# Performance work log

Hardware: AMD Instinct MI355X
Metric: run time of the kernel (lower is better)

## Reference

```python
import jax, jax.numpy as jnp
import numpy as np

N, E, D_IN, H, D_OUT = 50000, 1600000, 256, 128, 64


def setup_inputs() -> dict:
    key = jax.random.key(0)
    ks = jax.random.split(key, 8)
    x = jax.random.normal(ks[0], (N, D_IN), dtype=jnp.float32)
    edge_index = jax.random.randint(ks[1], (2, E), 0, N, dtype=jnp.int64)
    W1 = jax.random.normal(ks[2], (D_IN, H), dtype=jnp.float32) / np.float32(np.sqrt(D_IN))
    b1 = jnp.zeros((H,), jnp.float32)
    W2 = jax.random.normal(ks[3], (H, H), dtype=jnp.float32) / np.float32(np.sqrt(H))
    b2 = jnp.zeros((H,), jnp.float32)
    W3 = jax.random.normal(ks[4], (H, D_OUT), dtype=jnp.float32) / np.float32(np.sqrt(H))
    b3 = jnp.zeros((D_OUT,), jnp.float32)
    return {"x": x, "W1": W1, "b1": b1, "W2": W2, "b2": b2, "W3": W3, "b3": b3,
            "edge_index": edge_index}


def reference(x, W1, b1, W2, b2, W3, b3, edge_index):
    n = x.shape[0]
    # GCN: add self-loops, symmetric normalization D^{-1/2}(A+I)D^{-1/2}
    loop = jnp.arange(n, dtype=edge_index.dtype)
    src = jnp.concatenate([edge_index[0], loop])
    dst = jnp.concatenate([edge_index[1], loop])
    deg = jax.ops.segment_sum(jnp.ones_like(dst, x.dtype), dst, num_segments=n)
    dinv = jnp.where(deg > 0, jax.lax.rsqrt(deg), 0.0).astype(x.dtype)
    norm = dinv[src] * dinv[dst]  # [E+N]

    def gcn_layer(h, W, b):
        h = h @ W                                   # [N, F_out]
        msg = norm[:, None] * h[src]                # gather + scale, [E+N, F_out]
        return jax.ops.segment_sum(msg, dst, num_segments=n) + b

    h = jax.nn.relu(gcn_layer(x, W1, b1))
    h = jax.nn.relu(gcn_layer(h, W2, b2))
    return gcn_layer(h, W3, b3)
```

## Files before the change

kernel.cpp:

```cpp
#include <hip/hip_runtime.h>


constexpr int DIN = 256;
constexpr int HID = 128;
constexpr int DOUT = 64;
constexpr int MAXB = 1024;
constexpr int BSH = 6;
constexpr int EPB = 8192;

typedef unsigned short ushort_t;
typedef unsigned int uint_t;
typedef __attribute__((ext_vector_type(8))) short bf16x8;
typedef __attribute__((ext_vector_type(4))) float f32x4;

__device__ inline ushort_t f2bf(float f) {
  uint_t u = __float_as_uint(f);
  u += 0x7FFF + ((u >> 16) & 1);
  return (ushort_t)(u >> 16);
}
__device__ inline float bf2f(ushort_t b) {
  return __uint_as_float(((uint_t)b) << 16);
}

template <int SH>
__device__ inline uint_t ldrow32(const ushort_t* __restrict__ t, int c, uint_t lb) {
  return *(const uint_t*)((const char*)t + ((((uint_t)c) << SH) | lb));
}


__device__ inline void wprep_one(const float* __restrict__ W, ushort_t* __restrict__ Bhi,
                                 ushort_t* __restrict__ Blo, int K, int F, int i) {
  int k = i / F, nn = i % F;
  int t = nn >> 4, s = k >> 5, q = (k >> 3) & 3, j = k & 7;
  int lane = q * 16 + (nn & 15);
  int KS = K >> 5;
  size_t idx = (((size_t)t * KS + s) * 64 + (size_t)lane) * 8 + j;
  float w = W[i];
  ushort_t h = f2bf(w);
  float r = w - bf2f(h);
  Bhi[idx] = h;
  Blo[idx] = f2bf(r);
}


__global__ __launch_bounds__(256) void initprep_kernel(
    int* __restrict__ bucket_total, int iblocks,
    const float* __restrict__ W1, ushort_t* __restrict__ W1hi, ushort_t* __restrict__ W1lo,
    const float* __restrict__ W2, ushort_t* __restrict__ W2hi, ushort_t* __restrict__ W2lo,
    const float* __restrict__ W3, ushort_t* __restrict__ W3hi, ushort_t* __restrict__ W3lo) {
  if ((int)blockIdx.x < iblocks) {
    int i = blockIdx.x * 256 + threadIdx.x;
    if (i < MAXB) bucket_total[i] = 0;
  } else {
    int idx = ((int)blockIdx.x - iblocks) * 256 + threadIdx.x;
    constexpr int S1 = DIN * HID;
    constexpr int S2 = S1 + HID * HID;
    constexpr int S3 = S2 + HID * DOUT;
    if (idx < S1) wprep_one(W1, W1hi, W1lo, DIN, HID, idx);
    else if (idx < S2) wprep_one(W2, W2hi, W2lo, HID, HID, idx - S1);
    else if (idx < S3) wprep_one(W3, W3hi, W3lo, HID, DOUT, idx - S2);
  }
}


__global__ __launch_bounds__(256) void bin_kernel(const int* __restrict__ dst, int e,
    int nbuckets, int* __restrict__ bucket_total, int* __restrict__ block_base) {
  __shared__ int h[MAXB];
  int tid = threadIdx.x;
  for (int i = tid; i < nbuckets; i += 256) h[i] = 0;
  __syncthreads();
  int base = blockIdx.x * EPB;
  int end = min(base + EPB, e);
  for (int i = base + tid; i < end; i += 256) atomicAdd(&h[dst[i] >> BSH], 1);
  __syncthreads();
  for (int i = tid; i < nbuckets; i += 256) {
    int v = h[i];
    if (v) block_base[(size_t)blockIdx.x * nbuckets + i] = atomicAdd(&bucket_total[i], v);
  }
}


__global__ __launch_bounds__(256) void scan_buckets_kernel(const int* __restrict__ total,
    int* __restrict__ base, int nb) {
  __shared__ int sums[256];
  int t = threadIdx.x;
  int a[4];
  int ls = 0;
#pragma unroll
  for (int k = 0; k < 4; ++k) {
    int idx = t * 4 + k;
    a[k] = (idx < nb) ? total[idx] : 0;
    ls += a[k];
  }
  sums[t] = ls;
  __syncthreads();
  for (int off = 1; off < 256; off <<= 1) {
    int u = (t >= off) ? sums[t - off] : 0;
    __syncthreads();
    sums[t] += u;
    __syncthreads();
  }
  int run = sums[t] - ls;
#pragma unroll
  for (int k = 0; k < 4; ++k) {
    int idx = t * 4 + k;
    if (idx < nb) base[idx] = run;
    run += a[k];
  }
  if (t == 255) base[nb] = sums[255];
}


template <int K, int F, bool SCALE>
__device__ inline void gemm_mfma_dev(const float* __restrict__ X,
    const ushort_t* __restrict__ Bhi, const ushort_t* __restrict__ Blo,
    const float* __restrict__ dinv, ushort_t* __restrict__ T, int n, int bid) {
  constexpr int NT = F / 16;
  constexpr int KS = K / 32;
  int wave = threadIdx.x >> 6;
  int lane = threadIdx.x & 63;
  int q = lane >> 4;
  int m = lane & 15;
  int arow = bid * 64 + wave * 16 + m;
  bool valid = arow < n;
  const float* xrow = X + (size_t)arow * K;

  f32x4 acc[NT];
#pragma unroll
  for (int t = 0; t < NT; ++t) acc[t] = (f32x4){0.f, 0.f, 0.f, 0.f};

  for (int s = 0; s < KS; ++s) {
    float av[8];
    if (valid) {
      float4 u0 = *(const float4*)(xrow + s * 32 + q * 8);
      float4 u1 = *(const float4*)(xrow + s * 32 + q * 8 + 4);
      av[0] = u0.x; av[1] = u0.y; av[2] = u0.z; av[3] = u0.w;
      av[4] = u1.x; av[5] = u1.y; av[6] = u1.z; av[7] = u1.w;
    } else {
#pragma unroll
      for (int j = 0; j < 8; ++j) av[j] = 0.f;
    }
    bf16x8 ahi, alo;
#pragma unroll
    for (int j = 0; j < 8; ++j) {
      ushort_t h = f2bf(av[j]);
      ahi[j] = (short)h;
      alo[j] = (short)f2bf(av[j] - bf2f(h));
    }
#pragma unroll
    for (int t = 0; t < NT; ++t) {
      size_t boff = (((size_t)t * KS + s) * 64 + (size_t)lane) * 8;
      bf16x8 bh = *(const bf16x8*)(Bhi + boff);
      bf16x8 bl = *(const bf16x8*)(Blo + boff);
      acc[t] = __builtin_amdgcn_mfma_f32_16x16x32_bf16(ahi, bh, acc[t], 0, 0, 0);
      acc[t] = __builtin_amdgcn_mfma_f32_16x16x32_bf16(alo, bh, acc[t], 0, 0, 0);
      acc[t] = __builtin_amdgcn_mfma_f32_16x16x32_bf16(ahi, bl, acc[t], 0, 0, 0);
    }
  }

  int orow_base = bid * 64 + wave * 16 + q * 4;
#pragma unroll
  for (int r = 0; r < 4; ++r) {
    int orow = orow_base + r;
    if (orow >= n) continue;
    float sc = SCALE ? dinv[orow] : 1.0f;
    ushort_t* trow = T + (size_t)orow * F + m;
#pragma unroll
    for (int t = 0; t < NT; ++t) trow[t * 16] = f2bf(sc * acc[t][r]);
  }
}


__global__ __launch_bounds__(256) void fusedA2_kernel(
    const float* __restrict__ X, const ushort_t* __restrict__ Bhi,
    const ushort_t* __restrict__ Blo, ushort_t* __restrict__ T, int n, int gblocks,
    const int* __restrict__ src, const int* __restrict__ dst,
    const int* __restrict__ bucket_base, const int* __restrict__ block_base,
    uint_t* __restrict__ binned, int e, int nbuckets) {
  if ((int)blockIdx.x < gblocks) {
    gemm_mfma_dev<DIN, HID, false>(X, Bhi, Blo, nullptr, T, n, blockIdx.x);
  } else {
    __shared__ int rkh[MAXB];
    __shared__ int cbase[MAXB];
    int tid = threadIdx.x;
    int blk = (int)blockIdx.x - gblocks;
    for (int i = tid; i < nbuckets; i += 256) {
      rkh[i] = 0;
      cbase[i] = bucket_base[i] + block_base[(size_t)blk * nbuckets + i];
    }
    __syncthreads();
    int base = blk * EPB;
    int end = min(base + EPB, e);
    for (int i = base + tid; i < end; i += 256) {
      int d = dst[i];
      int s = src[i];
      int b = d >> BSH;
      int r = atomicAdd(&rkh[b], 1);
      binned[cbase[b] + r] = ((uint_t)d << 16) | (uint_t)s;
    }
  }
}


__global__ __launch_bounds__(256) void csr_kernel(const uint_t* __restrict__ binned,
    const int* __restrict__ bucket_base, int n, int* __restrict__ row_start,
    int* __restrict__ deg, float* __restrict__ dinv, int* __restrict__ col,
    ushort_t* __restrict__ Ta) {
  __shared__ int cnt[64];
  __shared__ int rk[64];
  __shared__ int rs[64];
  __shared__ float sdinv[64];
  __shared__ int ebs[2];
  int tid = threadIdx.x;
  int b = blockIdx.x;
  int node0 = b << BSH;
  if (tid < 64) { cnt[tid] = 0; rk[tid] = 0; }
  if (tid == 0) { ebs[0] = bucket_base[b]; ebs[1] = bucket_base[b + 1]; }
  __syncthreads();
  int ebase = ebs[0];
  int esz = ebs[1] - ebase;
  for (int i = tid; i < esz; i += 256)
    atomicAdd(&cnt[(int)(binned[ebase + i] >> 16) - node0], 1);
  __syncthreads();
  if (tid < 64) {
    int v = cnt[tid];
    int inc = v;
#pragma unroll
    for (int off = 1; off < 64; off <<= 1) {
      int u = __shfl_up(inc, off, 64);
      if (tid >= off) inc += u;
    }
    rs[tid] = inc - v;
    float di = rsqrtf((float)(v + 1));
    sdinv[tid] = di;
    int node = node0 + tid;
    if (node < n) {
      deg[node] = v + 1;
      dinv[node] = di;
      row_start[node] = ebase + (inc - v);
    }
  }
  __syncthreads();
  for (int i = tid; i < esz; i += 256) {
    uint_t p = binned[ebase + i];
    int l = (int)(p >> 16) - node0;
    int r = atomicAdd(&rk[l], 1);
    col[ebase + rs[l] + r] = (int)(p & 0xFFFFu);
  }
  int nrows = min(64, n - node0);
  if (nrows > 0) {
    uint4* tw = (uint4*)Ta + ((size_t)node0 << 4);
    int nv4 = nrows << 4;
    for (int i = tid; i < nv4; i += 256) {
      float sc = sdinv[i >> 4];
      uint4 w = tw[i];
      uint_t ww[4] = {w.x, w.y, w.z, w.w};
#pragma unroll
      for (int j = 0; j < 4; ++j) {
        float lo = sc * bf2f((ushort_t)(ww[j] & 0xFFFF));
        float hi = sc * bf2f((ushort_t)(ww[j] >> 16));
        ww[j] = (uint_t)f2bf(lo) | ((uint_t)f2bf(hi) << 16);
      }
      w.x = ww[0]; w.y = ww[1]; w.z = ww[2]; w.w = ww[3];
      tw[i] = w;
    }
  }
}


template <int FOUT>
__global__ __launch_bounds__(256) void spmm_gemm_kernel(
    const ushort_t* __restrict__ t, const int* __restrict__ row_start,
    const int* __restrict__ deg, const int* __restrict__ col,
    const float* __restrict__ dinv, const float* __restrict__ bias,
    const ushort_t* __restrict__ Bhi, const ushort_t* __restrict__ Blo,
    ushort_t* __restrict__ Tout, int n) {
  constexpr int FIN = 128;
  constexpr int NPB = 8;
  constexpr int LDW = FIN + 4;
  __shared__ float agg[16][LDW];
  int wave = threadIdx.x >> 6;
  int lane = threadIdx.x & 63;
  int tid = threadIdx.x;
  int nb0 = (int)blockIdx.x * NPB;
  uint_t lb = (uint_t)lane << 2;

  {
    float* z = &agg[8][0];
    for (int i = tid; i < 8 * LDW; i += 256) z[i] = 0.f;
  }

  {
    int ln0 = wave * 2;
    int n0 = nb0 + ln0;
    int n1 = n0 + 1;
    bool h0 = n0 < n, h1 = n1 < n;
    int rs0 = h0 ? row_start[n0] : 0, e0 = h0 ? deg[n0] - 1 : 0;
    int rs1 = h1 ? row_start[n1] : 0, e1 = h1 ? deg[n1] - 1 : 0;
    float di0 = h0 ? dinv[n0] : 0.f;
    float di1 = h1 ? dinv[n1] : 0.f;
    float bx = bias[2 * lane], by = bias[2 * lane + 1];
    float ax0 = 0.f, ay0 = 0.f, ax1 = 0.f, ay1 = 0.f;
    if (h0) {
      uint_t s0 = ldrow32<8>(t, n0, lb);
      ax0 = bf2f((ushort_t)(s0 & 0xFFFF)); ay0 = bf2f((ushort_t)(s0 >> 16));
    }
    if (h1) {
      uint_t s1 = ldrow32<8>(t, n1, lb);
      ax1 = bf2f((ushort_t)(s1 & 0xFFFF)); ay1 = bf2f((ushort_t)(s1 >> 16));
    }
    int p0 = rs0, q0 = rs0 + e0;
    int p1 = rs1, q1 = rs1 + e1;
    while (p0 + 8 <= q0 && p1 + 8 <= q1) {
      int c[16];
      uint_t v[16];
#pragma unroll
      for (int j = 0; j < 8; ++j) { c[j] = col[p0 + j]; c[8 + j] = col[p1 + j]; }
#pragma unroll
      for (int j = 0; j < 16; ++j) v[j] = ldrow32<8>(t, c[j], lb);
#pragma unroll
      for (int j = 0; j < 8; ++j) {
        ax0 += bf2f((ushort_t)(v[j] & 0xFFFF));
        ay0 += bf2f((ushort_t)(v[j] >> 16));
        ax1 += bf2f((ushort_t)(v[8 + j] & 0xFFFF));
        ay1 += bf2f((ushort_t)(v[8 + j] >> 16));
      }
      p0 += 8; p1 += 8;
    }
    while (p0 + 4 <= q0 && p1 + 4 <= q1) {
      int c[8];
      uint_t v[8];
#pragma unroll
      for (int j = 0; j < 4; ++j) { c[j] = col[p0 + j]; c[4 + j] = col[p1 + j]; }
#pragma unroll
      for (int j = 0; j < 8; ++j) v[j] = ldrow32<8>(t, c[j], lb);
#pragma unroll
      for (int j = 0; j < 4; ++j) {
        ax0 += bf2f((ushort_t)(v[j] & 0xFFFF));
        ay0 += bf2f((ushort_t)(v[j] >> 16));
        ax1 += bf2f((ushort_t)(v[4 + j] & 0xFFFF));
        ay1 += bf2f((ushort_t)(v[4 + j] >> 16));
      }
      p0 += 4; p1 += 4;
    }
    for (; p0 + 4 <= q0; p0 += 4) {
      int c[4]; uint_t v[4];
#pragma unroll
      for (int j = 0; j < 4; ++j) c[j] = col[p0 + j];
#pragma unroll
      for (int j = 0; j < 4; ++j) v[j] = ldrow32<8>(t, c[j], lb);
#pragma unroll
      for (int j = 0; j < 4; ++j) {
        ax0 += bf2f((ushort_t)(v[j] & 0xFFFF)); ay0 += bf2f((ushort_t)(v[j] >> 16));
      }
    }
    for (; p0 < q0; ++p0) {
      uint_t v = ldrow32<8>(t, col[p0], lb);
      ax0 += bf2f((ushort_t)(v & 0xFFFF)); ay0 += bf2f((ushort_t)(v >> 16));
    }
    for (; p1 + 4 <= q1; p1 += 4) {
      int c[4]; uint_t v[4];
#pragma unroll
      for (int j = 0; j < 4; ++j) c[j] = col[p1 + j];
#pragma unroll
      for (int j = 0; j < 4; ++j) v[j] = ldrow32<8>(t, c[j], lb);
#pragma unroll
      for (int j = 0; j < 4; ++j) {
        ax1 += bf2f((ushort_t)(v[j] & 0xFFFF)); ay1 += bf2f((ushort_t)(v[j] >> 16));
      }
    }
    for (; p1 < q1; ++p1) {
      uint_t v = ldrow32<8>(t, col[p1], lb);
      ax1 += bf2f((ushort_t)(v & 0xFFFF)); ay1 += bf2f((ushort_t)(v >> 16));
    }
    float2 o0, o1;
    o0.x = h0 ? fmaxf(fmaf(di0, ax0, bx), 0.f) : 0.f;
    o0.y = h0 ? fmaxf(fmaf(di0, ay0, by), 0.f) : 0.f;
    o1.x = h1 ? fmaxf(fmaf(di1, ax1, bx), 0.f) : 0.f;
    o1.y = h1 ? fmaxf(fmaf(di1, ay1, by), 0.f) : 0.f;
    *(float2*)&agg[ln0][2 * lane] = o0;
    *(float2*)&agg[ln0 + 1][2 * lane] = o1;
  }
  __syncthreads();

  constexpr int NT = FOUT / 16;
  constexpr int KS = FIN / 32;
  constexpr int NTW = NT / 4;
  int q = lane >> 4, m = lane & 15;
  f32x4 acc[NTW];
#pragma unroll
  for (int tt = 0; tt < NTW; ++tt) acc[tt] = (f32x4){0.f, 0.f, 0.f, 0.f};
  const float* arow = &agg[m][0];
#pragma unroll
  for (int s = 0; s < KS; ++s) {
    float4 u0 = *(const float4*)(arow + s * 32 + q * 8);
    float4 u1 = *(const float4*)(arow + s * 32 + q * 8 + 4);
    float av[8];
    av[0] = u0.x; av[1] = u0.y; av[2] = u0.z; av[3] = u0.w;
    av[4] = u1.x; av[5] = u1.y; av[6] = u1.z; av[7] = u1.w;
    bf16x8 ahi, alo;
#pragma unroll
    for (int j = 0; j < 8; ++j) {
      ushort_t h = f2bf(av[j]);
      ahi[j] = (short)h;
      alo[j] = (short)f2bf(av[j] - bf2f(h));
    }
#pragma unroll
    for (int tt = 0; tt < NTW; ++tt) {
      int tg = wave * NTW + tt;
      size_t boff = (((size_t)tg * KS + s) * 64 + (size_t)lane) * 8;
      bf16x8 bh = *(const bf16x8*)(Bhi + boff);
      bf16x8 bl = *(const bf16x8*)(Blo + boff);
      acc[tt] = __builtin_amdgcn_mfma_f32_16x16x32_bf16(ahi, bh, acc[tt], 0, 0, 0);
      acc[tt] = __builtin_amdgcn_mfma_f32_16x16x32_bf16(alo, bh, acc[tt], 0, 0, 0);
      acc[tt] = __builtin_amdgcn_mfma_f32_16x16x32_bf16(ahi, bl, acc[tt], 0, 0, 0);
    }
  }
#pragma unroll
  for (int r = 0; r < 4; ++r) {
    int row = q * 4 + r;
    if (row >= NPB) continue;
    int orow = nb0 + row;
    if (orow >= n) continue;
    float sc = dinv[orow];
    ushort_t* trow = Tout + (size_t)orow * FOUT + m;
#pragma unroll
    for (int tt = 0; tt < NTW; ++tt)
      trow[(wave * NTW + tt) * 16] = f2bf(sc * acc[tt][r]);
  }
}


__global__ __launch_bounds__(256) void spmm64_kernel(const ushort_t* __restrict__ t,
    const int* __restrict__ row_start, const int* __restrict__ deg,
    const int* __restrict__ col, const float* __restrict__ dinv,
    const float* __restrict__ bias, float* __restrict__ out, int n) {
  int gw = (int)((blockIdx.x * 256u + threadIdx.x) >> 6);
  int lane = threadIdx.x & 63;
  int half = lane >> 5;
  int hl = lane & 31;
  int n0 = gw * 2;
  if (n0 >= n) return;
  int node = n0 + half;
  bool valid = node < n;
  int vnode = valid ? node : n0;
  int rs = row_start[vnode];
  int e  = valid ? (deg[vnode] - 1) : 0;
  float di = dinv[vnode];
  uint_t lb = (uint_t)hl << 2;

  uint_t su = ldrow32<7>(t, vnode, lb);
  float ax = bf2f((ushort_t)(su & 0xFFFF));
  float ay = bf2f((ushort_t)(su >> 16));

  for (int k = 0; k < e; k += 8) {
    int c[8];
    uint_t v[8];
#pragma unroll
    for (int j = 0; j < 8; ++j) c[j] = col[(k + j) < e ? (rs + k + j) : rs];
#pragma unroll
    for (int j = 0; j < 8; ++j) v[j] = ldrow32<7>(t, c[j], lb);
#pragma unroll
    for (int j = 0; j < 8; ++j) {
      if ((k + j) < e) {
        ax += bf2f((ushort_t)(v[j] & 0xFFFF));
        ay += bf2f((ushort_t)(v[j] >> 16));
      }
    }
  }
  if (valid) {
    float bx = bias[2 * hl], by = bias[2 * hl + 1];
    ax = fmaf(di, ax, bx);
    ay = fmaf(di, ay, by);
    float2 o;
    o.x = ax;
    o.y = ay;
    *(float2*)(out + (size_t)node * DOUT + 2 * hl) = o;
  }
}


extern "C" void kernel_launch(void* const* d_in, const int* in_sizes, int n_in,
                              void* d_out, int out_size, void* d_ws, size_t ws_size,
                              hipStream_t stream) {
  const float* x  = (const float*)d_in[0];
  const float* W1 = (const float*)d_in[1];
  const float* b1 = (const float*)d_in[2];
  const float* W2 = (const float*)d_in[3];
  const float* b2 = (const float*)d_in[4];
  const float* W3 = (const float*)d_in[5];
  const float* b3 = (const float*)d_in[6];
  const int* ei   = (const int*)d_in[7];

  int n = in_sizes[0] / DIN;
  int e = in_sizes[7] / 2;
  const int* src = ei;
  const int* dst = ei + e;

  char* ws = (char*)d_ws;
  size_t off = 0;
  auto alloc = [&](size_t bytes) -> void* {
    off = (off + 255) & ~(size_t)255;
    void* p = ws + off;
    off += bytes;
    return p;
  };
  int nbuckets = (n + 63) >> BSH;
  int nbin = (e + EPB - 1) / EPB;

  int*      bucket_total = (int*)alloc((size_t)MAXB * 4);
  int*      bucket_base  = (int*)alloc((size_t)(MAXB + 1) * 4);
  int*      block_base   = (int*)alloc((size_t)nbin * nbuckets * 4);
  uint_t*   binned       = (uint_t*)alloc((size_t)e * 4);
  int*      deg          = (int*)alloc((size_t)n * 4);
  float*    dinv         = (float*)alloc((size_t)n * 4);
  int*      row_start    = (int*)alloc((size_t)n * 4);
  int*      col          = (int*)alloc((size_t)e * 4);
  ushort_t* Ta           = (ushort_t*)alloc((size_t)n * HID * 2);
  ushort_t* Tb           = (ushort_t*)alloc((size_t)n * HID * 2);
  ushort_t* W1hi         = (ushort_t*)alloc((size_t)DIN * HID * 2);
  ushort_t* W1lo         = (ushort_t*)alloc((size_t)DIN * HID * 2);
  ushort_t* W2hi         = (ushort_t*)alloc((size_t)HID * HID * 2);
  ushort_t* W2lo         = (ushort_t*)alloc((size_t)HID * HID * 2);
  ushort_t* W3hi         = (ushort_t*)alloc((size_t)HID * DOUT * 2);
  ushort_t* W3lo         = (ushort_t*)alloc((size_t)HID * DOUT * 2);
  (void)ws_size;

  int gemm_blocks = (n + 63) / 64;
  int sg_blocks = (n + 7) / 8;
  int nwaves = (n + 1) / 2;
  int spmm_blocks = (nwaves + 3) / 4;
  constexpr int WPREP_TOTAL = DIN * HID + HID * HID + HID * DOUT;
  int wblocks = (WPREP_TOTAL + 255) / 256;
  int iblocks = MAXB / 256;

  initprep_kernel<<<iblocks + wblocks, 256, 0, stream>>>(
      bucket_total, iblocks,
      W1, W1hi, W1lo, W2, W2hi, W2lo, W3, W3hi, W3lo);
  bin_kernel<<<nbin, 256, 0, stream>>>(dst, e, nbuckets, bucket_total, block_base);
  scan_buckets_kernel<<<1, 256, 0, stream>>>(bucket_total, bucket_base, nbuckets);
  fusedA2_kernel<<<gemm_blocks + nbin, 256, 0, stream>>>(
      x, W1hi, W1lo, Ta, n, gemm_blocks,
      src, dst, bucket_base, block_base, binned, e, nbuckets);
  csr_kernel<<<nbuckets, 256, 0, stream>>>(binned, bucket_base, n, row_start,
                                           deg, dinv, col, Ta);

  spmm_gemm_kernel<HID><<<sg_blocks, 256, 0, stream>>>(
      Ta, row_start, deg, col, dinv, b1, W2hi, W2lo, Tb, n);
  spmm_gemm_kernel<DOUT><<<sg_blocks, 256, 0, stream>>>(
      Tb, row_start, deg, col, dinv, b2, W3hi, W3lo, Ta, n);
  spmm64_kernel<<<spmm_blocks, 256, 0, stream>>>(
      Ta, row_start, deg, col, dinv, b3, (float*)d_out, n);
}
```

Measured before the change: 333.8 us.

## Aggregate 16 nodes per 512-thread block to fill MFMA tiles

Result: no change. 332.5 us (-0.4%).

```diff
diff --git a/kernel.cpp b/kernel.cpp
--- a/kernel.cpp
+++ b/kernel.cpp
@@ -269,26 +269,20 @@
 
 
 template <int FOUT>
-__global__ __launch_bounds__(256) void spmm_gemm_kernel(
+__global__ __launch_bounds__(512) void spmm_gemm_kernel(
     const ushort_t* __restrict__ t, const int* __restrict__ row_start,
     const int* __restrict__ deg, const int* __restrict__ col,
     const float* __restrict__ dinv, const float* __restrict__ bias,
     const ushort_t* __restrict__ Bhi, const ushort_t* __restrict__ Blo,
     ushort_t* __restrict__ Tout, int n) {
   constexpr int FIN = 128;
-  constexpr int NPB = 8;
+  constexpr int NPB = 16;
   constexpr int LDW = FIN + 4;
-  __shared__ float agg[16][LDW];
+  __shared__ float agg[NPB][LDW];
   int wave = threadIdx.x >> 6;
   int lane = threadIdx.x & 63;
-  int tid = threadIdx.x;
   int nb0 = (int)blockIdx.x * NPB;
   uint_t lb = (uint_t)lane << 2;
-
-  {
-    float* z = &agg[8][0];
-    for (int i = tid; i < 8 * LDW; i += 256) z[i] = 0.f;
-  }
 
   {
     int ln0 = wave * 2;
@@ -385,48 +379,38 @@
 
   constexpr int NT = FOUT / 16;
   constexpr int KS = FIN / 32;
-  constexpr int NTW = NT / 4;
-  int q = lane >> 4, m = lane & 15;
-  f32x4 acc[NTW];
-#pragma unroll
-  for (int tt = 0; tt < NTW; ++tt) acc[tt] = (f32x4){0.f, 0.f, 0.f, 0.f};
-  const float* arow = &agg[m][0];
-#pragma unroll
-  for (int s = 0; s < KS; ++s) {
-    float4 u0 = *(const float4*)(arow + s * 32 + q * 8);
-    float4 u1 = *(const float4*)(arow + s * 32 + q * 8 + 4);
-    float av[8];
-    av[0] = u0.x; av[1] = u0.y; av[2] = u0.z; av[3] = u0.w;
-    av[4] = u1.x; av[5] = u1.y; av[6] = u1.z; av[7] = u1.w;
-    bf16x8 ahi, alo;
-#pragma unroll
-    for (int j = 0; j < 8; ++j) {
-      ushort_t h = f2bf(av[j]);
-      ahi[j] = (short)h;
-      alo[j] = (short)f2bf(av[j] - bf2f(h));
-    }
-#pragma unroll
-    for (int tt = 0; tt < NTW; ++tt) {
-      int tg = wave * NTW + tt;
-      size_t boff = (((size_t)tg * KS + s) * 64 + (size_t)lane) * 8;
+  if (wave < NT) {
+    int q = lane >> 4, m = lane & 15;
+    f32x4 acc = (f32x4){0.f, 0.f, 0.f, 0.f};
+    const float* arow = &agg[m][0];
+#pragma unroll
+    for (int s = 0; s < KS; ++s) {
+      float4 u0 = *(const float4*)(arow + s * 32 + q * 8);
+      float4 u1 = *(const float4*)(arow + s * 32 + q * 8 + 4);
+      float av[8];
+      av[0] = u0.x; av[1] = u0.y; av[2] = u0.z; av[3] = u0.w;
+      av[4] = u1.x; av[5] = u1.y; av[6] = u1.z; av[7] = u1.w;
+      bf16x8 ahi, alo;
+#pragma unroll
+      for (int j = 0; j < 8; ++j) {
+        ushort_t h = f2bf(av[j]);
+        ahi[j] = (short)h;
+        alo[j] = (short)f2bf(av[j] - bf2f(h));
+      }
+      size_t boff = (((size_t)wave * KS + s) * 64 + (size_t)lane) * 8;
       bf16x8 bh = *(const bf16x8*)(Bhi + boff);
       bf16x8 bl = *(const bf16x8*)(Blo + boff);
-      acc[tt] = __builtin_amdgcn_mfma_f32_16x16x32_bf16(ahi, bh, acc[tt], 0, 0, 0);
-      acc[tt] = __builtin_amdgcn_mfma_f32_16x16x32_bf16(alo, bh, acc[tt], 0, 0, 0);
-      acc[tt] = __builtin_amdgcn_mfma_f32_16x16x32_bf16(ahi, bl, acc[tt], 0, 0, 0);
-    }
-  }
-#pragma unroll
-  for (int r = 0; r < 4; ++r) {
-    int row = q * 4 + r;
-    if (row >= NPB) continue;
-    int orow = nb0 + row;
-    if (orow >= n) continue;
-    float sc = dinv[orow];
-    ushort_t* trow = Tout + (size_t)orow * FOUT + m;
-#pragma unroll
-    for (int tt = 0; tt < NTW; ++tt)
-      trow[(wave * NTW + tt) * 16] = f2bf(sc * acc[tt][r]);
+      acc = __builtin_amdgcn_mfma_f32_16x16x32_bf16(ahi, bh, acc, 0, 0, 0);
+      acc = __builtin_amdgcn_mfma_f32_16x16x32_bf16(alo, bh, acc, 0, 0, 0);
+      acc = __builtin_amdgcn_mfma_f32_16x16x32_bf16(ahi, bl, acc, 0, 0, 0);
+    }
+#pragma unroll
+    for (int r = 0; r < 4; ++r) {
+      int orow = nb0 + q * 4 + r;
+      if (orow >= n) continue;
+      float sc = dinv[orow];
+      Tout[(size_t)orow * FOUT + wave * 16 + m] = f2bf(sc * acc[r]);
+    }
   }
 }
 
@@ -527,7 +511,7 @@
   (void)ws_size;
 
   int gemm_blocks = (n + 63) / 64;
-  int sg_blocks = (n + 7) / 8;
+  int sg_blocks = (n + 15) / 16;
   int nwaves = (n + 1) / 2;
   int spmm_blocks = (nwaves + 3) / 4;
   constexpr int WPREP_TOTAL = DIN * HID + HID * HID + HID * DOUT;
@@ -545,9 +529,9 @@
   csr_kernel<<<nbuckets, 256, 0, stream>>>(binned, bucket_base, n, row_start,
                                            deg, dinv, col, Ta);
 
-  spmm_gemm_kernel<HID><<<sg_blocks, 256, 0, stream>>>(
+  spmm_gemm_kernel<HID><<<sg_blocks, 512, 0, stream>>>(
       Ta, row_start, deg, col, dinv, b1, W2hi, W2lo, Tb, n);
-  spmm_gemm_kernel<DOUT><<<sg_blocks, 256, 0, stream>>>(
+  spmm_gemm_kernel<DOUT><<<sg_blocks, 512, 0, stream>>>(
       Tb, row_start, deg, col, dinv, b2, W3hi, W3lo, Ta, n);
   spmm64_kernel<<<spmm_blocks, 256, 0, stream>>>(
       Ta, row_start, deg, col, dinv, b3, (float*)d_out, n);
```
